# Kernel optimization log

Measured on AMD Instinct MI355X. Metric: run time of the kernel, lower is better.

## Reference

```python
import jax, jax.numpy as jnp
import numpy as np

E = 1024   # embed_dim
H = 16     # num_heads
NQ = 8     # ffn_dim == n_qubits
B, S = 2, 2048


def setup_inputs() -> dict:
    key = jax.random.key(0)
    ks = jax.random.split(key, 8)
    g = lambda k, sh, sc=1.0: jax.random.normal(k, sh, jnp.float32) * sc
    return {
        "x": g(ks[0], (B, S, E)),
        "w_qkv": g(ks[1], (3 * E, E), 0.02),      # nn.Linear(E, 3E, bias=False).weight
        "w_comb": g(ks[2], (E, E), 0.02),          # combine Linear weight
        "b_comb": jnp.zeros((E,), jnp.float32),
        "gamma1": jnp.ones((E,), jnp.float32),     # norm1
        "beta1": jnp.zeros((E,), jnp.float32),
        "gamma2": jnp.ones((E,), jnp.float32),     # norm2
        "beta2": jnp.zeros((E,), jnp.float32),
        "theta": g(ks[3], (NQ,)),                  # trainable RY angles
        "w1": g(ks[4], (1, NQ), 0.3),              # linear1 weight [1, n_qubits]
        "b1": jnp.zeros((1,), jnp.float32),
    }


def _layernorm(x, g, b, eps=1e-5):
    m = jnp.mean(x, axis=-1, keepdims=True)
    v = jnp.var(x, axis=-1, keepdims=True)
    return (x - m) * jax.lax.rsqrt(v + eps) * g + b


def reference(x, w_qkv, w_comb, b_comb, gamma1, beta1, gamma2, beta2, theta, w1, b1):
    Bx, Sx, Em = x.shape
    dk = Em // H
    # ---- attention ----
    qkv = (x @ w_qkv.T).reshape(Bx, Sx, 3, H, dk)
    q = jnp.transpose(qkv[:, :, 0], (0, 2, 1, 3))  # [B,H,S,dk]
    k = jnp.transpose(qkv[:, :, 1], (0, 2, 1, 3))
    v = jnp.transpose(qkv[:, :, 2], (0, 2, 1, 3))
    scores = jnp.einsum('bhqd,bhkd->bhqk', q, k) / jnp.sqrt(jnp.float32(dk))
    probs = jax.nn.softmax(scores, axis=-1)        # dropout = identity (eval)
    out = jnp.einsum('bhqk,bhkd->bhqd', probs, v)
    out = jnp.transpose(out, (0, 2, 1, 3)).reshape(Bx, Sx, Em)
    attn = out @ w_comb.T + b_comb
    x1 = _layernorm(x + attn, gamma1, beta1)
    # ---- quantum FFN: RX(x_i) encode, RY(theta_i), <Z_i> = cos(theta_i)*cos(x_i) ----
    z = jnp.cos(x1[..., :theta.shape[0]]) * jnp.cos(theta)  # [B,S,NQ]
    ffn = z @ w1.T + b1                                      # [B,S,1], broadcasts
    return _layernorm(x1 + ffn, gamma2, beta2)
```

## Files before the change

### kernel.cpp

```cpp
#include <hip/hip_runtime.h>
#include <hip/hip_bf16.h>
#include <math.h>

typedef __bf16 bf16;
typedef bf16 bf16x8 __attribute__((ext_vector_type(8)));
typedef float f32x4 __attribute__((ext_vector_type(4)));
typedef unsigned int u32;

#define EMB 1024
#define NH 16
#define DK 64
#define SEQ 2048
#define NB 2
#define NTOK (NB*SEQ)

#define QSCALE 0.18033688011112043f

#if defined(__has_builtin)
#if __has_builtin(__builtin_amdgcn_exp2f)
#define EXP2(x) __builtin_amdgcn_exp2f(x)
#else
#define EXP2(x) exp2f(x)
#endif
#else
#define EXP2(x) exp2f(x)
#endif

__device__ __forceinline__ void gl_lds16(const void* g, void* l) {
    __builtin_amdgcn_global_load_lds(
        (const __attribute__((address_space(1))) u32*)g,
        (__attribute__((address_space(3))) u32*)l, 16, 0, 0);
}

#define SWZ(row, colblk) (((row)*64) + ((((colblk) ^ ((row)&7)))*8))

#define PSTR 72

__global__ __launch_bounds__(256) void convert3(
    const float* __restrict__ s0, const float* __restrict__ s1,
    const float* __restrict__ s2,
    bf16* __restrict__ d0, bf16* __restrict__ d1, bf16* __restrict__ d2)
{
    const float* src; bf16* dst; int n;
    switch (blockIdx.y) {
        case 0:  src = s0; dst = d0; n = NTOK*EMB;  break;
        case 1:  src = s1; dst = d1; n = 3*EMB*EMB; break;
        default: src = s2; dst = d2; n = EMB*EMB;   break;
    }
    int i = (blockIdx.x * 256 + threadIdx.x) * 4;
    if (i + 3 < n) {
        float4 v = *(const float4*)(src + i);
        dst[i+0] = (bf16)v.x; dst[i+1] = (bf16)v.y;
        dst[i+2] = (bf16)v.z; dst[i+3] = (bf16)v.w;
    }
}

template<int MODE, int BM>
__global__ __launch_bounds__(256) void gemm_bt(
    const bf16* __restrict__ Aa, const bf16* __restrict__ Bb,
    bf16* __restrict__ qb, bf16* __restrict__ kb, bf16* __restrict__ vtb,
    float* __restrict__ outc, int Kdim)
{
    constexpr int MI = BM / 32;
    __shared__ __align__(16) bf16 At[BM*64];
    __shared__ __align__(16) bf16 Bt[128*64];
    const int tid  = threadIdx.x;
    const int w    = tid >> 6, lane = tid & 63;
    const int quad = lane >> 4, l15 = lane & 15;
    const int wr   = w >> 1,   wc  = w & 1;
    const int m0 = blockIdx.y * BM, n0 = blockIdx.x * 128;
    const int lrow = lane >> 3;
    const int lswz = ((lane & 7) ^ lrow) * 8;

    f32x4 acc[MI][4] = {};

    for (int k0 = 0; k0 < Kdim; k0 += 64) {
        __syncthreads();
        for (int i = 0; i < MI; ++i) {
            int r = w*(BM/4) + i*8 + lrow;
            gl_lds16(Aa + (size_t)(m0 + r)*Kdim + k0 + lswz, At + (w*(BM/4) + i*8)*64);
        }
        for (int i = 0; i < 4; ++i) {
            int r = w*32 + i*8 + lrow;
            gl_lds16(Bb + (size_t)(n0 + r)*Kdim + k0 + lswz, Bt + (w*32 + i*8)*64);
        }
        __syncthreads();
        for (int kk = 0; kk < 2; ++kk) {
            bf16x8 a[MI], b[4];
            for (int i = 0; i < MI; ++i) {
                int row = wr*(BM/2) + i*16 + l15;
                a[i] = *(const bf16x8*)(At + SWZ(row, 4*kk + quad));
            }
            for (int j = 0; j < 4; ++j) {
                int row = wc*64 + j*16 + l15;
                b[j] = *(const bf16x8*)(Bt + SWZ(row, 4*kk + quad));
            }
            for (int i = 0; i < MI; ++i)
                for (int j = 0; j < 4; ++j)
                    acc[i][j] = __builtin_amdgcn_mfma_f32_16x16x32_bf16(a[i], b[j], acc[i][j], 0, 0, 0);
        }
    }

    for (int i = 0; i < MI; ++i) for (int j = 0; j < 4; ++j) {
        int rb  = m0 + wr*(BM/2) + i*16 + quad*4;
        int col = n0 + wc*64 + j*16 + l15;
        if (MODE == 0) {
            int c = col >> 10, h = (col >> 6) & 15, d = col & 63;
            int b_ = rb >> 11, s = rb & 2047;
            int bh = b_*NH + h;
            if (c == 2) {
                bf16 tmp[4] __attribute__((aligned(8)));
                for (int r = 0; r < 4; ++r) tmp[r] = (bf16)acc[i][j][r];
                *(ushort4*)(vtb + ((size_t)bh*DK + d)*SEQ + s) = *(ushort4*)tmp;
            } else if (c == 0) {
                for (int r = 0; r < 4; ++r)
                    qb[((size_t)bh*SEQ + s + r)*DK + d] = (bf16)(acc[i][j][r] * QSCALE);
            } else {
                for (int r = 0; r < 4; ++r)
                    kb[((size_t)bh*SEQ + s + r)*DK + d] = (bf16)acc[i][j][r];
            }
        } else {
            for (int r = 0; r < 4; ++r)
                outc[(size_t)(rb + r)*EMB + col] = acc[i][j][r];
        }
    }
}

__global__ __launch_bounds__(256) void attn_kernel(
    const bf16* __restrict__ q, const bf16* __restrict__ k,
    const bf16* __restrict__ vt, bf16* __restrict__ out)
{
    __shared__ __align__(16) bf16 QP[4*32*PSTR];
    __shared__ __align__(16) bf16 Kt[64*64];
    __shared__ __align__(16) bf16 Vt[64*64];

    const int tid  = threadIdx.x;
    const int w    = tid >> 6, lane = tid & 63;
    const int quad = lane >> 4, l15 = lane & 15;
    const int bh = blockIdx.y, qt = blockIdx.x;
    const int lrow = lane >> 3;
    const int lswz = ((lane & 7) ^ lrow) * 8;

    for (int i = 0; i < 4; ++i) {
        int r = w*32 + i*8 + lrow;
        gl_lds16(q + ((size_t)bh*SEQ + qt*128 + r)*DK + lswz, QP + (w*32 + i*8)*64);
    }
    asm volatile("s_waitcnt vmcnt(0)" ::: "memory");

    bf16x8 qf[2][2];
    for (int rt = 0; rt < 2; ++rt)
        for (int kk = 0; kk < 2; ++kk)
            qf[rt][kk] = *(const bf16x8*)(QP + SWZ(w*32 + rt*16 + l15, 4*kk + quad));

    bf16* Pw = QP + w * 32 * PSTR;

    f32x4 O[2][4] = {};
    float psum[2][4] = {};

    for (int kt = 0; kt < SEQ/64; ++kt) {
        __syncthreads();
        for (int i = 0; i < 2; ++i) {
            int r = w*16 + i*8 + lrow;
            gl_lds16(k  + ((size_t)bh*SEQ + kt*64 + r)*DK + lswz, Kt + (w*16 + i*8)*64);
            gl_lds16(vt + ((size_t)bh*DK + r)*SEQ + kt*64 + lswz, Vt + (w*16 + i*8)*64);
        }
        __syncthreads();

        f32x4 sc[2][4] = {};
        for (int kk = 0; kk < 2; ++kk)
            for (int j = 0; j < 4; ++j) {
                bf16x8 b = *(const bf16x8*)(Kt + SWZ(j*16 + l15, 4*kk + quad));
                for (int rt = 0; rt < 2; ++rt)
                    sc[rt][j] = __builtin_amdgcn_mfma_f32_16x16x32_bf16(qf[rt][kk], b, sc[rt][j], 0, 0, 0);
            }

        for (int rt = 0; rt < 2; ++rt)
            for (int j = 0; j < 4; ++j)
                for (int r = 0; r < 4; ++r) {
                    float p = EXP2(sc[rt][j][r]);
                    psum[rt][r] += p;
                    Pw[(rt*16 + quad*4 + r)*PSTR + j*16 + l15] = (bf16)p;
                }

        asm volatile("s_waitcnt lgkmcnt(0)" ::: "memory");

        for (int kk = 0; kk < 2; ++kk) {
            bf16x8 vb[4];
            for (int j = 0; j < 4; ++j)
                vb[j] = *(const bf16x8*)(Vt + SWZ(j*16 + l15, 4*kk + quad));
            for (int rt = 0; rt < 2; ++rt) {
                bf16x8 a = *(const bf16x8*)(Pw + (rt*16 + l15)*PSTR + kk*32 + quad*8);
                for (int j = 0; j < 4; ++j)
                    O[rt][j] = __builtin_amdgcn_mfma_f32_16x16x32_bf16(a, vb[j], O[rt][j], 0, 0, 0);
            }
        }
    }

    for (int rt = 0; rt < 2; ++rt)
        for (int r = 0; r < 4; ++r) {
            float s = psum[rt][r];
            for (int m = 1; m < 16; m <<= 1) s += __shfl_xor(s, m, 64);
            psum[rt][r] = 1.f / s;
        }

    const int b_ = bh >> 4, h = bh & 15;
    for (int rt = 0; rt < 2; ++rt)
        for (int j = 0; j < 4; ++j)
            for (int r = 0; r < 4; ++r) {
                int t   = b_*SEQ + qt*128 + w*32 + rt*16 + quad*4 + r;
                int col = h*DK + j*16 + l15;
                out[(size_t)t*EMB + col] = (bf16)(O[rt][j][r] * psum[rt][r]);
            }
}

__global__ __launch_bounds__(256) void ln_kernel(
    const float* __restrict__ x, const float* __restrict__ comb,
    const float* __restrict__ bcomb,
    const float* __restrict__ g1, const float* __restrict__ be1,
    const float* __restrict__ g2, const float* __restrict__ be2,
    const float* __restrict__ theta, const float* __restrict__ w1v,
    const float* __restrict__ b1v, float* __restrict__ out)
{
    const int t = blockIdx.x, tid = threadIdx.x;
    __shared__ float red[8];
    __shared__ float fp2[2];
    const int e0 = tid*4;

    float4 xv = *(const float4*)(x    + (size_t)t*EMB + e0);
    float4 cv = *(const float4*)(comb + (size_t)t*EMB + e0);
    float4 bv = *(const float4*)(bcomb + e0);
    float r[4] = { xv.x + cv.x + bv.x, xv.y + cv.y + bv.y,
                   xv.z + cv.z + bv.z, xv.w + cv.w + bv.w };

    float s = 0.f, ss = 0.f;
    for (int i = 0; i < 4; ++i) { s += r[i]; ss += r[i]*r[i]; }
    for (int m = 1; m < 64; m <<= 1) { s += __shfl_xor(s, m, 64); ss += __shfl_xor(ss, m, 64); }
    if ((tid & 63) == 0) { red[(tid>>6)*2] = s; red[(tid>>6)*2+1] = ss; }
    __syncthreads();
    s  = red[0] + red[2] + red[4] + red[6];
    ss = red[1] + red[3] + red[5] + red[7];
    float mean = s * (1.f/1024.f);
    float var  = ss * (1.f/1024.f) - mean*mean;
    float inv  = rsqrtf(var + 1e-5f);
    float x1[4];
    for (int i = 0; i < 4; ++i) {
        int e = e0 + i;
        x1[i] = (r[i] - mean)*inv*g1[e] + be1[e];
    }
    __syncthreads();
    if (e0 < 8) {
        float pf = 0.f;
        for (int i = 0; i < 4; ++i) {
            int e = e0 + i;
            pf += cosf(x1[i]) * cosf(theta[e]) * w1v[e];
        }
        fp2[tid] = pf;
    }
    __syncthreads();
    float f = fp2[0] + fp2[1] + b1v[0];

    float s2 = 0.f, ss2 = 0.f;
    for (int i = 0; i < 4; ++i) { float v2 = x1[i] + f; s2 += v2; ss2 += v2*v2; }
    for (int m = 1; m < 64; m <<= 1) { s2 += __shfl_xor(s2, m, 64); ss2 += __shfl_xor(ss2, m, 64); }
    if ((tid & 63) == 0) { red[(tid>>6)*2] = s2; red[(tid>>6)*2+1] = ss2; }
    __syncthreads();
    s2  = red[0] + red[2] + red[4] + red[6];
    ss2 = red[1] + red[3] + red[5] + red[7];
    float mean2 = s2 * (1.f/1024.f);
    float var2  = ss2 * (1.f/1024.f) - mean2*mean2;
    float inv2  = rsqrtf(var2 + 1e-5f);
    float4 ov;
    ov.x = ((x1[0] + f) - mean2)*inv2*g2[e0+0] + be2[e0+0];
    ov.y = ((x1[1] + f) - mean2)*inv2*g2[e0+1] + be2[e0+1];
    ov.z = ((x1[2] + f) - mean2)*inv2*g2[e0+2] + be2[e0+2];
    ov.w = ((x1[3] + f) - mean2)*inv2*g2[e0+3] + be2[e0+3];
    *(float4*)(out + (size_t)t*EMB + e0) = ov;
}

extern "C" void kernel_launch(void* const* d_in, const int* in_sizes, int n_in,
                              void* d_out, int out_size, void* d_ws, size_t ws_size,
                              hipStream_t stream)
{
    const float* x      = (const float*)d_in[0];
    const float* w_qkv  = (const float*)d_in[1];
    const float* w_comb = (const float*)d_in[2];
    const float* b_comb = (const float*)d_in[3];
    const float* g1     = (const float*)d_in[4];
    const float* be1    = (const float*)d_in[5];
    const float* g2     = (const float*)d_in[6];
    const float* be2    = (const float*)d_in[7];
    const float* theta  = (const float*)d_in[8];
    const float* w1v    = (const float*)d_in[9];
    const float* b1v    = (const float*)d_in[10];
    float* out = (float*)d_out;

    char* ws = (char*)d_ws;
    bf16*  xb     = (bf16*)(ws);
    bf16*  wqkvb  = (bf16*)(ws + ( 8u<<20));
    bf16*  wcombb = (bf16*)(ws + (14u<<20));
    bf16*  qb     = (bf16*)(ws + (16u<<20));
    bf16*  kb     = (bf16*)(ws + (24u<<20));
    bf16*  vtb    = (bf16*)(ws + (32u<<20));
    bf16*  attn   = (bf16*)(ws + (40u<<20));
    float* comb   = (float*)(ws + (16u<<20));

    convert3<<<dim3(4096, 3), 256, 0, stream>>>(x, w_qkv, w_comb, xb, wqkvb, wcombb);

    gemm_bt<0,128><<<dim3(3*EMB/128, NTOK/128), 256, 0, stream>>>(
        xb, wqkvb, qb, kb, vtb, nullptr, EMB);
    attn_kernel<<<dim3(SEQ/128, NB*NH), 256, 0, stream>>>(qb, kb, vtb, attn);
    gemm_bt<1,64><<<dim3(EMB/128, NTOK/64), 256, 0, stream>>>(
        attn, wcombb, nullptr, nullptr, nullptr, comb, EMB);
    ln_kernel<<<NTOK, 256, 0, stream>>>(x, comb, b_comb, g1, be1, g2, be2,
                                        theta, w1v, b1v, out);
}
```

Measured before the change: 220.1 us.

## Read Q/K/V fragments directly from global memory and compute row sums via MFMA

```diff
diff --git a/kernel.cpp b/kernel.cpp
--- a/kernel.cpp
+++ b/kernel.cpp
@@ -130,87 +130,70 @@
     const bf16* __restrict__ q, const bf16* __restrict__ k,
     const bf16* __restrict__ vt, bf16* __restrict__ out)
 {
-    __shared__ __align__(16) bf16 QP[4*32*PSTR];
-    __shared__ __align__(16) bf16 Kt[64*64];
-    __shared__ __align__(16) bf16 Vt[64*64];
+    __shared__ __align__(16) bf16 P[4*32*PSTR];
 
     const int tid  = threadIdx.x;
     const int w    = tid >> 6, lane = tid & 63;
     const int quad = lane >> 4, l15 = lane & 15;
     const int bh = blockIdx.y, qt = blockIdx.x;
-    const int lrow = lane >> 3;
-    const int lswz = ((lane & 7) ^ lrow) * 8;
-
-    for (int i = 0; i < 4; ++i) {
-        int r = w*32 + i*8 + lrow;
-        gl_lds16(q + ((size_t)bh*SEQ + qt*128 + r)*DK + lswz, QP + (w*32 + i*8)*64);
-    }
-    asm volatile("s_waitcnt vmcnt(0)" ::: "memory");
+
+    const bf16* qp = q  + (size_t)bh*SEQ*DK;
+    const bf16* kp = k  + (size_t)bh*SEQ*DK;
+    const bf16* vp = vt + (size_t)bh*DK*SEQ;
 
     bf16x8 qf[2][2];
     for (int rt = 0; rt < 2; ++rt)
         for (int kk = 0; kk < 2; ++kk)
-            qf[rt][kk] = *(const bf16x8*)(QP + SWZ(w*32 + rt*16 + l15, 4*kk + quad));
-
-    bf16* Pw = QP + w * 32 * PSTR;
+            qf[rt][kk] = *(const bf16x8*)(qp + (size_t)(qt*128 + w*32 + rt*16 + l15)*DK + kk*32 + quad*8);
+
+    bf16* Pw = P + w * 32 * PSTR;
+
+    bf16x8 ones;
+    for (int i = 0; i < 8; ++i) ones[i] = (bf16)1.0f;
 
     f32x4 O[2][4] = {};
-    float psum[2][4] = {};
+    f32x4 ps[2] = {};
 
     for (int kt = 0; kt < SEQ/64; ++kt) {
-        __syncthreads();
-        for (int i = 0; i < 2; ++i) {
-            int r = w*16 + i*8 + lrow;
-            gl_lds16(k  + ((size_t)bh*SEQ + kt*64 + r)*DK + lswz, Kt + (w*16 + i*8)*64);
-            gl_lds16(vt + ((size_t)bh*DK + r)*SEQ + kt*64 + lswz, Vt + (w*16 + i*8)*64);
-        }
-        __syncthreads();
-
         f32x4 sc[2][4] = {};
         for (int kk = 0; kk < 2; ++kk)
             for (int j = 0; j < 4; ++j) {
-                bf16x8 b = *(const bf16x8*)(Kt + SWZ(j*16 + l15, 4*kk + quad));
+                bf16x8 b = *(const bf16x8*)(kp + (size_t)(kt*64 + j*16 + l15)*DK + kk*32 + quad*8);
                 for (int rt = 0; rt < 2; ++rt)
                     sc[rt][j] = __builtin_amdgcn_mfma_f32_16x16x32_bf16(qf[rt][kk], b, sc[rt][j], 0, 0, 0);
             }
 
         for (int rt = 0; rt < 2; ++rt)
             for (int j = 0; j < 4; ++j)
-                for (int r = 0; r < 4; ++r) {
-                    float p = EXP2(sc[rt][j][r]);
-                    psum[rt][r] += p;
-                    Pw[(rt*16 + quad*4 + r)*PSTR + j*16 + l15] = (bf16)p;
-                }
+                for (int r = 0; r < 4; ++r)
+                    Pw[(rt*16 + quad*4 + r)*PSTR + j*16 + l15] = (bf16)EXP2(sc[rt][j][r]);
 
         asm volatile("s_waitcnt lgkmcnt(0)" ::: "memory");
 
         for (int kk = 0; kk < 2; ++kk) {
             bf16x8 vb[4];
             for (int j = 0; j < 4; ++j)
-                vb[j] = *(const bf16x8*)(Vt + SWZ(j*16 + l15, 4*kk + quad));
+                vb[j] = *(const bf16x8*)(vp + (size_t)(j*16 + l15)*SEQ + kt*64 + kk*32 + quad*8);
             for (int rt = 0; rt < 2; ++rt) {
                 bf16x8 a = *(const bf16x8*)(Pw + (rt*16 + l15)*PSTR + kk*32 + quad*8);
+                ps[rt] = __builtin_amdgcn_mfma_f32_16x16x32_bf16(a, ones, ps[rt], 0, 0, 0);
                 for (int j = 0; j < 4; ++j)
                     O[rt][j] = __builtin_amdgcn_mfma_f32_16x16x32_bf16(a, vb[j], O[rt][j], 0, 0, 0);
             }
         }
     }
 
-    for (int rt = 0; rt < 2; ++rt)
-        for (int r = 0; r < 4; ++r) {
-            float s = psum[rt][r];
-            for (int m = 1; m < 16; m <<= 1) s += __shfl_xor(s, m, 64);
-            psum[rt][r] = 1.f / s;
-        }
-
     const int b_ = bh >> 4, h = bh & 15;
-    for (int rt = 0; rt < 2; ++rt)
+    for (int rt = 0; rt < 2; ++rt) {
+        float inv[4];
+        for (int r = 0; r < 4; ++r) inv[r] = 1.f / ps[rt][r];
         for (int j = 0; j < 4; ++j)
             for (int r = 0; r < 4; ++r) {
                 int t   = b_*SEQ + qt*128 + w*32 + rt*16 + quad*4 + r;
                 int col = h*DK + j*16 + l15;
-                out[(size_t)t*EMB + col] = (bf16)(O[rt][j][r] * psum[rt][r]);
-            }
+                out[(size_t)t*EMB + col] = (bf16)(O[rt][j][r] * inv[r]);
+            }
+    }
 }
 
 __global__ __launch_bounds__(256) void ln_kernel(
```

Measured after the change: 299.7 us. 1.36x slower.
